# Performance work log

Hardware: AMD Instinct MI355X
Metric: run time of the kernel (lower is better)

Reference implementation:

```python
import jax, jax.numpy as jnp
import numpy as np

N = 1_000_000
IN_DIM = 128
OUT_DIM = 128
NUM_SEGMENTS = 16384
EPS = 1e-5


def setup_inputs() -> dict:
    key = jax.random.key(0)
    k1, k2, k3, k4, k5 = jax.random.split(key, 5)
    x = jax.random.normal(k1, (N, IN_DIM), dtype=jnp.float32)
    batch = jnp.sort(jax.random.randint(k2, (N,), 0, NUM_SEGMENTS, dtype=jnp.int64))
    # Linear params (Kaiming-ish uniform like torch default)
    bound = 1.0 / np.sqrt(IN_DIM)
    W = jax.random.uniform(k3, (OUT_DIM, IN_DIM), dtype=jnp.float32, minval=-bound, maxval=bound)
    b = jax.random.uniform(k4, (OUT_DIM,), dtype=jnp.float32, minval=-bound, maxval=bound)
    # LayerNorm affine params
    ln_w = jnp.ones((OUT_DIM,), dtype=jnp.float32)
    ln_b = jnp.zeros((OUT_DIM,), dtype=jnp.float32)
    return {"x": x, "batch": batch, "W": W, "b": b, "ln_w": ln_w, "ln_b": ln_b}


def reference(x, batch, W, b, ln_w, ln_b):
    # Linear: [N, IN] @ [IN, OUT] + b
    h = jnp.einsum('ni,oi->no', x, W) + b
    # LayerNorm over last dim
    mean = jnp.mean(h, axis=-1, keepdims=True)
    var = jnp.mean(jnp.square(h - mean), axis=-1, keepdims=True)
    h = (h - mean) * jax.lax.rsqrt(var + EPS) * ln_w + ln_b
    # scatter mean over segment ids (torch_scatter: sum / clamp(count, 1))
    seg_sum = jax.ops.segment_sum(h, batch, num_segments=NUM_SEGMENTS)
    count = jax.ops.segment_sum(jnp.ones((h.shape[0],), dtype=h.dtype), batch,
                                num_segments=NUM_SEGMENTS)
    out = seg_sum / jnp.maximum(count, 1.0)[:, None]
    return out
```

## Files before the change

kernel.cpp:

```cpp
#include <hip/hip_runtime.h>
#include <hip/hip_bf16.h>

#define NROWS 1000000
#define DIM 128
#define NSEG 16384
#define TILE_M 32
#define NT (NROWS / TILE_M)
#define XH_STRIDE 136
#define GRID1 768
#define EPSV 1e-5f

typedef __bf16 bf16x8 __attribute__((ext_vector_type(8)));
typedef __bf16 bf16x4 __attribute__((ext_vector_type(4)));
typedef float  f32x4  __attribute__((ext_vector_type(4)));

__global__ __launch_bounds__(256, 3)
void fused_lin_ln_scatter(const float* __restrict__ x,
                          const int*   __restrict__ batch,
                          const float* __restrict__ W,
                          const float* __restrict__ bias,
                          const float* __restrict__ lnw,
                          const float* __restrict__ lnb,
                          float* __restrict__ out) {
    __shared__ __align__(16) __bf16 xh[TILE_M * XH_STRIDE];
    __shared__ float2 stat2[2][TILE_M];
    __shared__ int    ibuf[TILE_M];

    const int t    = threadIdx.x;
    const int wave = t >> 6;
    const int lane = t & 63;
    const int q    = lane >> 4;
    const int l15  = lane & 15;
    const int rg   = wave >> 1;
    const int fh   = wave & 1;
    const int fbase = fh * 64;

    bf16x8 whf[4][4];
    #pragma unroll
    for (int nt = 0; nt < 4; ++nt) {
        const int f = fbase + nt * 16 + l15;
        #pragma unroll
        for (int ks = 0; ks < 4; ++ks) {
            const int k0 = ks * 32 + q * 8;
            const float4* wp = (const float4*)(W + f * DIM + k0);
            float4 a = wp[0], c = wp[1];
            float wv[8] = {a.x, a.y, a.z, a.w, c.x, c.y, c.z, c.w};
            bf16x8 hi;
            #pragma unroll
            for (int j = 0; j < 8; ++j) hi[j] = (__bf16)wv[j];
            whf[nt][ks] = hi;
        }
    }
    float bb[4], lwv[4], lbv[4];
    #pragma unroll
    for (int nt = 0; nt < 4; ++nt) {
        const int f = fbase + nt * 16 + l15;
        bb[nt]  = bias[f];
        lwv[nt] = lnw[f];
        lbv[nt] = lnb[f];
    }

    int it = blockIdx.x;
    float4 xr[4];
    int ibv = 0;
    {
        const float4* xp = (const float4*)(x + (size_t)it * TILE_M * DIM);
        #pragma unroll
        for (int j = 0; j < 4; ++j) xr[j] = xp[t + 256 * j];
        if (t < TILE_M) ibv = batch[it * TILE_M + t];
    }

    for (; it < NT; it += GRID1) {
        #pragma unroll
        for (int j = 0; j < 4; ++j) {
            const int idx = t + 256 * j;
            const int row = idx >> 5;
            const int c4  = (idx & 31) * 4;
            float4 v = xr[j];
            bf16x4 pk = {(__bf16)v.x, (__bf16)v.y, (__bf16)v.z, (__bf16)v.w};
            *(bf16x4*)&xh[row * XH_STRIDE + c4] = pk;
        }
        if (t < TILE_M) ibuf[t] = ibv;
        __syncthreads();

        const int s_first = ibuf[rg * 16];
        const int s_last  = ibuf[rg * 16 + 15];
        int sgr[4];
        #pragma unroll
        for (int r = 0; r < 4; ++r) sgr[r] = ibuf[rg * 16 + q * 4 + r];

        const int itn = it + GRID1;
        if (itn < NT) {
            const float4* xp = (const float4*)(x + (size_t)itn * TILE_M * DIM);
            #pragma unroll
            for (int j = 0; j < 4; ++j) xr[j] = xp[t + 256 * j];
            if (t < TILE_M) ibv = batch[itn * TILE_M + t];
        }

        f32x4 acc[4];
        #pragma unroll
        for (int nt = 0; nt < 4; ++nt)
            acc[nt] = (f32x4){bb[nt], bb[nt], bb[nt], bb[nt]};
        const int row_l = rg * 16 + l15;
        #pragma unroll
        for (int ks = 0; ks < 4; ++ks) {
            bf16x8 af = *(const bf16x8*)&xh[row_l * XH_STRIDE + ks * 32 + q * 8];
            #pragma unroll
            for (int nt = 0; nt < 4; ++nt)
                acc[nt] = __builtin_amdgcn_mfma_f32_16x16x32_bf16(af, whf[nt][ks], acc[nt], 0, 0, 0);
        }

        #pragma unroll
        for (int r = 0; r < 4; ++r) {
            float s  = acc[0][r] + acc[1][r] + acc[2][r] + acc[3][r];
            float sq = acc[0][r] * acc[0][r] + acc[1][r] * acc[1][r]
                     + acc[2][r] * acc[2][r] + acc[3][r] * acc[3][r];
            #pragma unroll
            for (int m = 1; m < 16; m <<= 1) {
                s  += __shfl_xor(s,  m, 64);
                sq += __shfl_xor(sq, m, 64);
            }
            if (l15 == 0)
                stat2[fh][rg * 16 + q * 4 + r] = make_float2(s, sq);
        }
        __syncthreads();

        float nv[4][4];
        #pragma unroll
        for (int r = 0; r < 4; ++r) {
            const int row = rg * 16 + q * 4 + r;
            float2 u0 = stat2[0][row], u1 = stat2[1][row];
            float mean = (u0.x + u1.x) * (1.0f / 128.0f);
            float var  = (u0.y + u1.y) * (1.0f / 128.0f) - mean * mean;
            float rs   = rsqrtf(var + EPSV);
            #pragma unroll
            for (int nt = 0; nt < 4; ++nt)
                nv[nt][r] = (acc[nt][r] - mean) * rs * lwv[nt] + lbv[nt];
        }

        if (s_first == s_last) {
            #pragma unroll
            for (int nt = 0; nt < 4; ++nt) {
                float v = nv[nt][0] + nv[nt][1] + nv[nt][2] + nv[nt][3];
                v += __shfl_xor(v, 16, 64);
                v += __shfl_xor(v, 32, 64);
                if (q == 0)
                    atomicAdd(out + (size_t)s_first * DIM + fbase + nt * 16 + l15, v);
            }
        } else {
            #pragma unroll
            for (int nt = 0; nt < 4; ++nt) {
                const int f = fbase + nt * 16 + l15;
                float a = nv[nt][0];
                #pragma unroll
                for (int r = 1; r < 4; ++r) {
                    if (sgr[r] != sgr[r - 1]) {
                        atomicAdd(out + (size_t)sgr[r - 1] * DIM + f, a);
                        a = 0.f;
                    }
                    a += nv[nt][r];
                }
                atomicAdd(out + (size_t)sgr[3] * DIM + f, a);
            }
        }
    }
}

__device__ __forceinline__ int lower_bound_seg(const int* __restrict__ batch, int v) {
    int lo = 0, hi = NROWS;
    while (lo < hi) {
        int m = (lo + hi) >> 1;
        if (batch[m] < v) lo = m + 1; else hi = m;
    }
    return lo;
}

__global__ __launch_bounds__(256)
void finalize_divide(float* __restrict__ out, const int* __restrict__ batch) {
    __shared__ float cnt[2];
    const int t = threadIdx.x;
    if (t < 2) {
        const int s = blockIdx.x * 2 + t;
        int c = lower_bound_seg(batch, s + 1) - lower_bound_seg(batch, s);
        cnt[t] = (float)max(c, 1);
    }
    __syncthreads();
    const size_t i = (size_t)blockIdx.x * 256 + t;
    out[i] = out[i] / cnt[t >> 7];
}

extern "C" void kernel_launch(void* const* d_in, const int* in_sizes, int n_in,
                              void* d_out, int out_size, void* d_ws, size_t ws_size,
                              hipStream_t stream) {
    const float* x     = (const float*)d_in[0];
    const int*   batch = (const int*)d_in[1];
    const float* W     = (const float*)d_in[2];
    const float* bias  = (const float*)d_in[3];
    const float* lnw   = (const float*)d_in[4];
    const float* lnb   = (const float*)d_in[5];
    float* out = (float*)d_out;

    hipMemsetAsync(out, 0, (size_t)out_size * sizeof(float), stream);
    fused_lin_ln_scatter<<<GRID1, 256, 0, stream>>>(x, batch, W, bias, lnw, lnb, out);
    finalize_divide<<<(NSEG * DIM) / 256, 256, 0, stream>>>(out, batch);
}
```

Baseline: 742.9 us.

## Double-buffer x tile prefetch two iterations ahead and batch finalize segment counts

The main kernel now holds two register sets of prefetched x tiles and batch ids and loads the tile two grid-strides ahead, so more global memory traffic is in flight while the current tile computes. The finalize kernel now handles 128 segments per block, finds segment boundaries with one binary search per boundary, and multiplies by a reciprocal count instead of dividing. This lowers redundant searches and launch work. The cost is doubled prefetch registers, which may pressure the 3-blocks-per-CU occupancy target.

```diff
diff --git a/kernel.cpp b/kernel.cpp
--- a/kernel.cpp
+++ b/kernel.cpp
@@ -60,107 +60,119 @@
         lbv[nt] = lnb[f];
     }
 
-    int it = blockIdx.x;
-    float4 xr[4];
-    int ibv = 0;
+    float4 xr[2][4];
+    int    ibv[2];
     {
-        const float4* xp = (const float4*)(x + (size_t)it * TILE_M * DIM);
+        const int it0 = blockIdx.x;
         #pragma unroll
-        for (int j = 0; j < 4; ++j) xr[j] = xp[t + 256 * j];
-        if (t < TILE_M) ibv = batch[it * TILE_M + t];
-    }
-
-    for (; it < NT; it += GRID1) {
+        for (int h = 0; h < 2; ++h) {
+            const float4* xp = (const float4*)(x + (size_t)(it0 + h * GRID1) * TILE_M * DIM);
+            #pragma unroll
+            for (int j = 0; j < 4; ++j) xr[h][j] = xp[t + 256 * j];
+        }
+        if (t < TILE_M) {
+            ibv[0] = batch[it0 * TILE_M + t];
+            ibv[1] = batch[(it0 + GRID1) * TILE_M + t];
+        }
+    }
+
+    for (int it = blockIdx.x; it < NT; it += 2 * GRID1) {
         #pragma unroll
-        for (int j = 0; j < 4; ++j) {
-            const int idx = t + 256 * j;
-            const int row = idx >> 5;
-            const int c4  = (idx & 31) * 4;
-            float4 v = xr[j];
-            bf16x4 pk = {(__bf16)v.x, (__bf16)v.y, (__bf16)v.z, (__bf16)v.w};
-            *(bf16x4*)&xh[row * XH_STRIDE + c4] = pk;
-        }
-        if (t < TILE_M) ibuf[t] = ibv;
-        __syncthreads();
-
-        const int s_first = ibuf[rg * 16];
-        const int s_last  = ibuf[rg * 16 + 15];
-        int sgr[4];
-        #pragma unroll
-        for (int r = 0; r < 4; ++r) sgr[r] = ibuf[rg * 16 + q * 4 + r];
-
-        const int itn = it + GRID1;
-        if (itn < NT) {
-            const float4* xp = (const float4*)(x + (size_t)itn * TILE_M * DIM);
-            #pragma unroll
-            for (int j = 0; j < 4; ++j) xr[j] = xp[t + 256 * j];
-            if (t < TILE_M) ibv = batch[itn * TILE_M + t];
-        }
-
-        f32x4 acc[4];
-        #pragma unroll
-        for (int nt = 0; nt < 4; ++nt)
-            acc[nt] = (f32x4){bb[nt], bb[nt], bb[nt], bb[nt]};
-        const int row_l = rg * 16 + l15;
-        #pragma unroll
-        for (int ks = 0; ks < 4; ++ks) {
-            bf16x8 af = *(const bf16x8*)&xh[row_l * XH_STRIDE + ks * 32 + q * 8];
+        for (int h = 0; h < 2; ++h) {
+            const int itc = it + h * GRID1;
+            if (itc >= NT) break;
+
+            #pragma unroll
+            for (int j = 0; j < 4; ++j) {
+                const int idx = t + 256 * j;
+                const int row = idx >> 5;
+                const int c4  = (idx & 31) * 4;
+                float4 v = xr[h][j];
+                bf16x4 pk = {(__bf16)v.x, (__bf16)v.y, (__bf16)v.z, (__bf16)v.w};
+                *(bf16x4*)&xh[row * XH_STRIDE + c4] = pk;
+            }
+            if (t < TILE_M) ibuf[t] = ibv[h];
+            __syncthreads();
+
+            const int s_first = ibuf[rg * 16];
+            const int s_last  = ibuf[rg * 16 + 15];
+            int sgr[4];
+            #pragma unroll
+            for (int r = 0; r < 4; ++r) sgr[r] = ibuf[rg * 16 + q * 4 + r];
+
+            const int itn = itc + 2 * GRID1;
+            if (itn < NT) {
+                const float4* xp = (const float4*)(x + (size_t)itn * TILE_M * DIM);
+                #pragma unroll
+                for (int j = 0; j < 4; ++j) xr[h][j] = xp[t + 256 * j];
+                if (t < TILE_M) ibv[h] = batch[itn * TILE_M + t];
+            }
+
+            f32x4 acc[4];
             #pragma unroll
             for (int nt = 0; nt < 4; ++nt)
-                acc[nt] = __builtin_amdgcn_mfma_f32_16x16x32_bf16(af, whf[nt][ks], acc[nt], 0, 0, 0);
-        }
-
-        #pragma unroll
-        for (int r = 0; r < 4; ++r) {
-            float s  = acc[0][r] + acc[1][r] + acc[2][r] + acc[3][r];
-            float sq = acc[0][r] * acc[0][r] + acc[1][r] * acc[1][r]
-                     + acc[2][r] * acc[2][r] + acc[3][r] * acc[3][r];
-            #pragma unroll
-            for (int m = 1; m < 16; m <<= 1) {
-                s  += __shfl_xor(s,  m, 64);
-                sq += __shfl_xor(sq, m, 64);
-            }
-            if (l15 == 0)
-                stat2[fh][rg * 16 + q * 4 + r] = make_float2(s, sq);
-        }
-        __syncthreads();
-
-        float nv[4][4];
-        #pragma unroll
-        for (int r = 0; r < 4; ++r) {
-            const int row = rg * 16 + q * 4 + r;
-            float2 u0 = stat2[0][row], u1 = stat2[1][row];
-            float mean = (u0.x + u1.x) * (1.0f / 128.0f);
-            float var  = (u0.y + u1.y) * (1.0f / 128.0f) - mean * mean;
-            float rs   = rsqrtf(var + EPSV);
-            #pragma unroll
-            for (int nt = 0; nt < 4; ++nt)
-                nv[nt][r] = (acc[nt][r] - mean) * rs * lwv[nt] + lbv[nt];
-        }
-
-        if (s_first == s_last) {
-            #pragma unroll
-            for (int nt = 0; nt < 4; ++nt) {
-                float v = nv[nt][0] + nv[nt][1] + nv[nt][2] + nv[nt][3];
-                v += __shfl_xor(v, 16, 64);
-                v += __shfl_xor(v, 32, 64);
-                if (q == 0)
-                    atomicAdd(out + (size_t)s_first * DIM + fbase + nt * 16 + l15, v);
-            }
-        } else {
-            #pragma unroll
-            for (int nt = 0; nt < 4; ++nt) {
-                const int f = fbase + nt * 16 + l15;
-                float a = nv[nt][0];
-                #pragma unroll
-                for (int r = 1; r < 4; ++r) {
-                    if (sgr[r] != sgr[r - 1]) {
-                        atomicAdd(out + (size_t)sgr[r - 1] * DIM + f, a);
-                        a = 0.f;
+                acc[nt] = (f32x4){bb[nt], bb[nt], bb[nt], bb[nt]};
+            const int row_l = rg * 16 + l15;
+            #pragma unroll
+            for (int ks = 0; ks < 4; ++ks) {
+                bf16x8 af = *(const bf16x8*)&xh[row_l * XH_STRIDE + ks * 32 + q * 8];
+                #pragma unroll
+                for (int nt = 0; nt < 4; ++nt)
+                    acc[nt] = __builtin_amdgcn_mfma_f32_16x16x32_bf16(af, whf[nt][ks], acc[nt], 0, 0, 0);
+            }
+
+            #pragma unroll
+            for (int r = 0; r < 4; ++r) {
+                float s  = acc[0][r] + acc[1][r] + acc[2][r] + acc[3][r];
+                float sq = acc[0][r] * acc[0][r] + acc[1][r] * acc[1][r]
+                         + acc[2][r] * acc[2][r] + acc[3][r] * acc[3][r];
+                #pragma unroll
+                for (int m = 1; m < 16; m <<= 1) {
+                    s  += __shfl_xor(s,  m, 64);
+                    sq += __shfl_xor(sq, m, 64);
+                }
+                if (l15 == 0)
+                    stat2[fh][rg * 16 + q * 4 + r] = make_float2(s, sq);
+            }
+            __syncthreads();
+
+            float nv[4][4];
+            #pragma unroll
+            for (int r = 0; r < 4; ++r) {
+                const int row = rg * 16 + q * 4 + r;
+                float2 u0 = stat2[0][row], u1 = stat2[1][row];
+                float mean = (u0.x + u1.x) * (1.0f / 128.0f);
+                float var  = (u0.y + u1.y) * (1.0f / 128.0f) - mean * mean;
+                float rs   = rsqrtf(var + EPSV);
+                #pragma unroll
+                for (int nt = 0; nt < 4; ++nt)
+                    nv[nt][r] = (acc[nt][r] - mean) * rs * lwv[nt] + lbv[nt];
+            }
+
+            if (s_first == s_last) {
+                #pragma unroll
+                for (int nt = 0; nt < 4; ++nt) {
+                    float v = nv[nt][0] + nv[nt][1] + nv[nt][2] + nv[nt][3];
+                    v += __shfl_xor(v, 16, 64);
+                    v += __shfl_xor(v, 32, 64);
+                    if (q == 0)
+                        atomicAdd(out + (size_t)s_first * DIM + fbase + nt * 16 + l15, v);
+                }
+            } else {
+                #pragma unroll
+                for (int nt = 0; nt < 4; ++nt) {
+                    const int f = fbase + nt * 16 + l15;
+                    float a = nv[nt][0];
+                    #pragma unroll
+                    for (int r = 1; r < 4; ++r) {
+                        if (sgr[r] != sgr[r - 1]) {
+                            atomicAdd(out + (size_t)sgr[r - 1] * DIM + f, a);
+                            a = 0.f;
+                        }
+                        a += nv[nt][r];
                     }
-                    a += nv[nt][r];
+                    atomicAdd(out + (size_t)sgr[3] * DIM + f, a);
                 }
-                atomicAdd(out + (size_t)sgr[3] * DIM + f, a);
             }
         }
     }
@@ -175,18 +187,26 @@
     return lo;
 }
 
+#define SEGS_PER_BLK 128
 __global__ __launch_bounds__(256)
 void finalize_divide(float* __restrict__ out, const int* __restrict__ batch) {
-    __shared__ float cnt[2];
-    const int t = threadIdx.x;
-    if (t < 2) {
-        const int s = blockIdx.x * 2 + t;
-        int c = lower_bound_seg(batch, s + 1) - lower_bound_seg(batch, s);
-        cnt[t] = (float)max(c, 1);
-    }
+    __shared__ int   bnd[SEGS_PER_BLK + 1];
+    __shared__ float rinv[SEGS_PER_BLK];
+    const int t  = threadIdx.x;
+    const int s0 = blockIdx.x * SEGS_PER_BLK;
+    if (t <= SEGS_PER_BLK) bnd[t] = lower_bound_seg(batch, s0 + t);
     __syncthreads();
-    const size_t i = (size_t)blockIdx.x * 256 + t;
-    out[i] = out[i] / cnt[t >> 7];
+    if (t < SEGS_PER_BLK) {
+        const int c = bnd[t + 1] - bnd[t];
+        rinv[t] = 1.0f / (float)max(c, 1);
+    }
+    __syncthreads();
+    float* base = out + (size_t)s0 * DIM;
+    #pragma unroll
+    for (int i = 0; i < (SEGS_PER_BLK * DIM) / 256; ++i) {
+        const int idx = t + 256 * i;
+        base[idx] *= rinv[idx >> 7];
+    }
 }
 
 extern "C" void kernel_launch(void* const* d_in, const int* in_sizes, int n_in,
@@ -202,5 +222,5 @@
 
     hipMemsetAsync(out, 0, (size_t)out_size * sizeof(float), stream);
     fused_lin_ln_scatter<<<GRID1, 256, 0, stream>>>(x, batch, W, bias, lnw, lnb, out);
-    finalize_divide<<<(NSEG * DIM) / 256, 256, 0, stream>>>(out, batch);
-}
+    finalize_divide<<<NSEG / SEGS_PER_BLK, 256, 0, stream>>>(out, batch);
+}
```

Result: slower. 776.4 us (+4.5%).
